# Kernel tuning notes

Hardware: AMD Instinct MI355X
Metric: run time of the kernel (lower is better)

Reference implementation:

```python
import jax, jax.numpy as jnp
import numpy as np

N_FFT = 1024
HOP = 256


def _hann(n):
    # torch.hann_window default is periodic
    return 0.5 * (1.0 - jnp.cos(2.0 * jnp.pi * jnp.arange(n) / n))


def _dft_kernel():
    # rfft(eye(n_fft)).T -> (n_fft//2+1, n_fft) complex, windowed along time axis
    win = _hann(N_FFT).astype(jnp.float32)
    dftm = jnp.fft.rfft(jnp.eye(N_FFT, dtype=jnp.float32), axis=-1).T * win[None, :]
    # rearrange 'f n ri -> (ri f) n': real rows first, then imag rows
    ker = jnp.concatenate([dftm.real, dftm.imag], axis=0)  # (2*(n_fft//2+1), n_fft)
    f2 = ker.shape[0]
    scale = jnp.ones((f2,), dtype=jnp.float32)
    scale = scale.at[1:(N_FFT + 1) // 2].set(2.0)   # positive freqs (real part), excl. DC & Nyquist
    scale = scale.at[(N_FFT + 2) // 2:].set(2.0)    # imag rows
    return (ker * scale[:, None] / N_FFT).astype(jnp.float32)  # (1026, 1024)


def setup_inputs() -> dict:
    key = jax.random.key(0)
    B, F, T = 16, N_FFT // 2 + 1, 1024
    x = jax.random.normal(key, (B, F, T, 2), dtype=jnp.float32)
    return {"x": x}


def reference(x) -> jnp.ndarray:
    # x: (B, freq, n_frames, 2)
    B, F, T, _ = x.shape
    # '... freq n ri -> ... (ri freq) n'
    xc = jnp.concatenate([x[..., 0], x[..., 1]], axis=1)  # (B, 2F, T)
    ker = _dft_kernel()                                   # (2F, n_fft)
    # conv_transpose1d(stride=hop) == per-frame GEMM then overlap-add
    frames = jnp.einsum('bct,cn->btn', xc, ker)           # (B, T, n_fft)
    L = (T - 1) * HOP + N_FFT
    idx = (jnp.arange(T)[:, None] * HOP + jnp.arange(N_FFT)[None, :]).reshape(-1)
    wav = jnp.zeros((B, L), dtype=x.dtype).at[:, idx].add(frames.reshape(B, -1))
    # COLA normalization: * hop / sum(window^2)
    win = _hann(N_FFT)
    coeff = (HOP / jnp.sum(win ** 2)).astype(x.dtype)
    return wav * coeff
```

## Files before the change

### kernel.cpp

```cpp
#include <hip/hip_runtime.h>
#include <hip/hip_bf16.h>

#define HOP 256
#define NB 16
#define NT 1024
#define MM (NB*NT)
#define LOUT ((NT-1)*HOP + 1024)
#define CQ (2.0f/(3.0f*1024.0f))
#define PACK_BLOCKS 2048

typedef __bf16 bf16x8 __attribute__((ext_vector_type(8)));
typedef float f32x4 __attribute__((ext_vector_type(4)));

__device__ __forceinline__ void gload_lds16(const void* g, void* l) {
  __builtin_amdgcn_global_load_lds(
      (const __attribute__((address_space(1))) void*)g,
      (__attribute__((address_space(3))) void*)l, 16, 0, 0);
}

__global__ void prep(const float* __restrict__ x, __hip_bfloat16* __restrict__ A,
                     __hip_bfloat16* __restrict__ B3, float* __restrict__ wint) {
  int tid = threadIdx.x;
  if (blockIdx.x >= PACK_BLOCKS) {
    int idx = (blockIdx.x - PACK_BLOCKS) * 256 + tid;
    int row = idx >> 9, c = idx & 511;
    int i = row & 255, nt = row >> 8;
    int oddh = i >> 7;
    int j = nt * 128 + (i & 127);
    int f, isSin;
    if (!oddh) {
      if (c < 257) { f = 2 * c; isSin = 0; } else { f = 2 * (c - 256); isSin = 1; }
    } else {
      if (c < 256) { f = 2 * c + 1; isSin = 0; } else { f = 2 * (c - 256) + 1; isSin = 1; }
    }
    const float w0 = 6.283185307179586f / 1024.f;
    int ph = (f * j) & 1023;
    float si, co;
    __sincosf((float)ph * w0, &si, &co);
    float sc = (f == 0 || f == 512) ? 1.f : 2.f;
    B3[idx] = __float2bfloat16(isSin ? -si * sc : co * sc);
    if (idx < 1024)
      wint[idx] = (0.5f - 0.5f * __cosf((float)idx * w0)) * CQ;
    return;
  }
  __shared__ float2 tile[64][65];
  int w = blockIdx.x;
  int b = w >> 7, fy = (w >> 4) & 7, tx = w & 15;
  int f0 = fy * 64, t0 = tx * 64;
  int tl = tid & 63, th = tid >> 6;
#pragma unroll
  for (int r = 0; r < 16; ++r) {
    int fl = r * 4 + th;
    tile[fl][tl] = *(const float2*)(x + (((size_t)b * 513 + f0 + fl) * 1024 + (t0 + tl)) * 2);
  }
  __syncthreads();
  int row = tid >> 2, s = tid & 3;
  float sp = 0.f;
  if (fy == 0 && s == 1)
    sp = x[(((size_t)b * 513 + 512) * 1024 + t0 + row) * 2];
  int cbase = (s & 1) * 256 + (s >> 1) * 512 + f0 / 2;
#pragma unroll
  for (int v = 0; v < 4; ++v) {
    bf16x8 pv;
#pragma unroll
    for (int u = 0; u < 8; ++u) {
      int e = v * 8 + u;
      float2 tv = tile[2 * e + (s >> 1)][row];
      float val = (s & 1) ? tv.y : tv.x;
      if (fy == 0 && s == 1 && e == 0) val = sp;
      pv[u] = (__bf16)val;
    }
    *(bf16x8*)(A + (size_t)(b * 1024 + t0 + row) * 1024 + cbase + v * 8) = pv;
  }
}

__global__ __launch_bounds__(512, 1) void gemm8(
    const __hip_bfloat16* __restrict__ A, const __hip_bfloat16* __restrict__ B3,
    const float* __restrict__ wint, __hip_bfloat16* __restrict__ C) {
  __shared__ __align__(16) __hip_bfloat16 smem[65536];
  int tid = threadIdx.x, lane = tid & 63, wv = tid >> 6;
  int wr = wv >> 2, wc = wv & 3;
  int nf = (blockIdx.x & 7) * 32 + (blockIdx.x >> 3);
  int M0 = (nf & 63) * 256;
  int nt = nf >> 6;
  int j0 = nt * 128;

  __hip_bfloat16* sA0 = smem;
  __hip_bfloat16* sA1 = smem + 16384;
  __hip_bfloat16* sB0 = smem + 32768;
  __hip_bfloat16* sB1 = smem + 40960;

  f32x4 accE[8][2] = {};
  f32x4 accO[8][2] = {};

#define SGA(KT, G, LB)                                                         \
  {                                                                            \
    int r_ = (G) * 64 + (tid >> 3);                                            \
    int s_ = (((tid & 7) ^ (r_ & 7)) * 8);                                     \
    gload_lds16(A + (size_t)(M0 + r_) * 1024 + (KT) * 64 + s_,                 \
                (LB) + (G) * 4096 + tid * 8);                                  \
  }
#define SGB(KT, G, LB)                                                         \
  {                                                                            \
    int r_ = (G) * 64 + (tid >> 3);                                            \
    int s_ = (((tid & 7) ^ (r_ & 7)) * 8);                                     \
    gload_lds16(B3 + (size_t)(nt * 256 + ((KT) >= 8 ? 128 : 0) + r_) * 512 +   \
                    ((KT) & 7) * 64 + s_,                                      \
                (LB) + (G) * 4096 + tid * 8);                                  \
  }
#define VMCNT(N) asm volatile("s_waitcnt vmcnt(" #N ")" ::: "memory")
#define BAR() __builtin_amdgcn_s_barrier()

#define LOADA(CA, P)                                                           \
  _Pragma("unroll") for (int jj = 0; jj < 4; ++jj) {                           \
    int row = wr * 128 + (P) * 64 + jj * 16 + (lane & 15);                     \
    _Pragma("unroll") for (int ks = 0; ks < 2; ++ks)                           \
        af[jj][ks] = *(const bf16x8*)&(CA)[row * 64 +                          \
            (((ks * 4 + (lane >> 4)) ^ (row & 7)) * 8)];                       \
  }
#define MFMAH(ACC, P)                                                          \
  __builtin_amdgcn_s_setprio(1);                                               \
  _Pragma("unroll") for (int jj = 0; jj < 4; ++jj)                             \
  _Pragma("unroll") for (int ks = 0; ks < 2; ++ks)                             \
  _Pragma("unroll") for (int ni = 0; ni < 2; ++ni)                             \
      ACC[(P) * 4 + jj][ni] = __builtin_amdgcn_mfma_f32_16x16x32_bf16(         \
          af[jj][ks], bfr[ks][ni], ACC[(P) * 4 + jj][ni], 0, 0, 0);            \
  __builtin_amdgcn_s_setprio(0);

#define TILE(CA, CB, NA, NBUF, K1, DOST, ACC)                                  \
  {                                                                            \
    bf16x8 bfr[2][2], af[4][2];                                                \
    _Pragma("unroll") for (int ni = 0; ni < 2; ++ni) {                         \
      int row = wc * 32 + ni * 16 + (lane & 15);                               \
      _Pragma("unroll") for (int ks = 0; ks < 2; ++ks)                         \
          bfr[ks][ni] = *(const bf16x8*)&(CB)[row * 64 +                       \
              (((ks * 4 + (lane >> 4)) ^ (row & 7)) * 8)];                     \
    }                                                                          \
    LOADA(CA, 0);                                                              \
    if (DOST) { SGB(K1, 0, NBUF); SGB(K1, 1, NBUF); }                          \
    BAR(); MFMAH(ACC, 0);                                                      \
    if (DOST) { VMCNT(2); } else { VMCNT(0); }                                 \
    BAR();                                                                     \
    LOADA(CA, 1);                                                              \
    if (DOST) { SGA(K1, 0, NA); SGA(K1, 2, NA); SGA(K1, 1, NA); SGA(K1, 3, NA); } \
    BAR(); MFMAH(ACC, 1);                                                      \
    if (DOST) { VMCNT(2); }                                                    \
    BAR();                                                                     \
  }

  SGB(0, 0, sB0); SGB(0, 1, sB0);
  SGA(0, 0, sA0); SGA(0, 2, sA0);
  SGA(0, 1, sA0); SGA(0, 3, sA0);
  VMCNT(2);
  BAR();

#pragma unroll
  for (int tt = 0; tt < 4; ++tt) {
    TILE(sA0, sB0, sA1, sB1, 2 * tt + 1, 1, accE);
    TILE(sA1, sB1, sA0, sB0, 2 * tt + 2, 1, accE);
  }
#pragma unroll
  for (int tt = 0; tt < 4; ++tt) {
    TILE(sA0, sB0, sA1, sB1, 2 * tt + 9, 1, accO);
    TILE(sA1, sB1, sA0, sB0, 2 * tt + 10, (tt < 3) ? 1 : 0, accO);
  }

  __hip_bfloat16* ct = smem;
  float wE[2], wO[2];
#pragma unroll
  for (int ni = 0; ni < 2; ++ni) {
    int jcol = j0 + wc * 32 + ni * 16 + (lane & 15);
    wE[ni] = wint[jcol];
    wO[ni] = wint[jcol + 512];
  }
#pragma unroll
  for (int mi = 0; mi < 8; ++mi) {
    int rbase = wr * 128 + mi * 16 + (lane >> 4) * 4;
#pragma unroll
    for (int ni = 0; ni < 2; ++ni) {
      int lc = wc * 32 + ni * 16 + (lane & 15);
#pragma unroll
      for (int r = 0; r < 4; ++r) {
        float E = accE[mi][ni][r], O = accO[mi][ni][r];
        ct[(rbase + r) * 256 + lc] = __float2bfloat16(wE[ni] * (E + O));
        ct[(rbase + r) * 256 + 128 + lc] = __float2bfloat16(wO[ni] * (E - O));
      }
    }
  }
  BAR();
#pragma unroll
  for (int k = 0; k < 16; ++k) {
    int row = k * 16 + (tid >> 5);
    int c0 = (tid & 31) * 8;
    int gcol = (c0 < 128) ? (j0 + c0) : (512 + j0 + c0 - 128);
    *(int4*)(C + (size_t)(M0 + row) * 1024 + gcol) = *(const int4*)&ct[row * 256 + c0];
  }
#undef SGA
#undef SGB
#undef VMCNT
#undef BAR
#undef LOADA
#undef MFMAH
#undef TILE
}

__global__ void ola2(const __hip_bfloat16* __restrict__ C, float* __restrict__ out) {
  int q = blockIdx.x;
  int b = blockIdx.y * 8 + (threadIdx.x >> 5);
  int r0 = (threadIdx.x & 31) * 8;
  size_t outl = (size_t)b * LOUT + q * 256 + r0;
  if (q >= 3 && q < 1024) {
    size_t mrow = ((size_t)b * 1024 + q) * 1024;
    bf16x8 v0 = *(const bf16x8*)&C[mrow + r0];
    bf16x8 v1 = *(const bf16x8*)&C[mrow - 1024 + 256 + r0];
    bf16x8 v2 = *(const bf16x8*)&C[mrow - 2048 + 512 + r0];
    bf16x8 v3 = *(const bf16x8*)&C[mrow - 3072 + 768 + r0];
    float res[8];
#pragma unroll
    for (int e = 0; e < 8; ++e)
      res[e] = (float)v0[e] + (float)v1[e] + (float)v2[e] + (float)v3[e];
    *(float4*)(out + outl) = make_float4(res[0], res[1], res[2], res[3]);
    *(float4*)(out + outl + 4) = make_float4(res[4], res[5], res[6], res[7]);
    return;
  }
#pragma unroll
  for (int e = 0; e < 8; ++e) {
    int l = q * 256 + r0 + e;
    int thi = l >> 8; if (thi > 1023) thi = 1023;
    int tlo = (l - 768) >> 8; if (tlo < 0) tlo = 0;
    float s = 0.f;
    for (int t = tlo; t <= thi; ++t)
      s += __bfloat162float(C[((size_t)b * 1024 + t) * 1024 + (l - (t << 8))]);
    out[outl + e] = s;
  }
}

extern "C" void kernel_launch(void* const* d_in, const int* in_sizes, int n_in,
                              void* d_out, int out_size, void* d_ws, size_t ws_size,
                              hipStream_t stream) {
  (void)in_sizes; (void)n_in; (void)out_size; (void)ws_size;
  const float* x = (const float*)d_in[0];
  float* out = (float*)d_out;
  char* ws = (char*)d_ws;
  size_t oA  = 0;
  size_t oB3 = oA + (size_t)MM * 1024 * 2;
  size_t oW  = oB3 + (size_t)1024 * 512 * 2;
  size_t oC  = oW + 1024 * 4;
  __hip_bfloat16* A  = (__hip_bfloat16*)(ws + oA);
  __hip_bfloat16* B3 = (__hip_bfloat16*)(ws + oB3);
  float* wint = (float*)(ws + oW);
  __hip_bfloat16* C  = (__hip_bfloat16*)(ws + oC);

  prep<<<dim3(PACK_BLOCKS + 2048), dim3(256), 0, stream>>>(x, A, B3, wint);
  gemm8<<<dim3(256), dim3(512), 0, stream>>>(A, B3, wint, C);
  ola2<<<dim3(1027, 2), dim3(256), 0, stream>>>(C, out);
}
```

Baseline: 64.11 us.

## Halve GEMM M-tile to 128 rows and launch 512 blocks with higher occupancy

```diff
diff --git a/kernel.cpp b/kernel.cpp
--- a/kernel.cpp
+++ b/kernel.cpp
@@ -74,24 +74,25 @@
   }
 }
 
-__global__ __launch_bounds__(512, 1) void gemm8(
+__global__ __launch_bounds__(512, 4) void gemm8(
     const __hip_bfloat16* __restrict__ A, const __hip_bfloat16* __restrict__ B3,
     const float* __restrict__ wint, __hip_bfloat16* __restrict__ C) {
-  __shared__ __align__(16) __hip_bfloat16 smem[65536];
+  __shared__ __align__(16) __hip_bfloat16 smem[32768];
   int tid = threadIdx.x, lane = tid & 63, wv = tid >> 6;
   int wr = wv >> 2, wc = wv & 3;
-  int nf = (blockIdx.x & 7) * 32 + (blockIdx.x >> 3);
-  int M0 = (nf & 63) * 256;
-  int nt = nf >> 6;
+  int q = blockIdx.x >> 3, xcd = blockIdx.x & 7;
+  int m_ = xcd + 8 * (q >> 2);
+  int nt = q & 3;
+  int M0 = m_ * 128;
   int j0 = nt * 128;
 
   __hip_bfloat16* sA0 = smem;
-  __hip_bfloat16* sA1 = smem + 16384;
-  __hip_bfloat16* sB0 = smem + 32768;
-  __hip_bfloat16* sB1 = smem + 40960;
-
-  f32x4 accE[8][2] = {};
-  f32x4 accO[8][2] = {};
+  __hip_bfloat16* sA1 = smem + 8192;
+  __hip_bfloat16* sB0 = smem + 16384;
+  __hip_bfloat16* sB1 = smem + 24576;
+
+  f32x4 accE[4][2] = {};
+  f32x4 accO[4][2] = {};
 
 #define SGA(KT, G, LB)                                                         \
   {                                                                            \
@@ -108,27 +109,13 @@
                     ((KT) & 7) * 64 + s_,                                      \
                 (LB) + (G) * 4096 + tid * 8);                                  \
   }
-#define VMCNT(N) asm volatile("s_waitcnt vmcnt(" #N ")" ::: "memory")
+#define VMCNT0() asm volatile("s_waitcnt vmcnt(0)" ::: "memory")
 #define BAR() __builtin_amdgcn_s_barrier()
-
-#define LOADA(CA, P)                                                           \
-  _Pragma("unroll") for (int jj = 0; jj < 4; ++jj) {                           \
-    int row = wr * 128 + (P) * 64 + jj * 16 + (lane & 15);                     \
-    _Pragma("unroll") for (int ks = 0; ks < 2; ++ks)                           \
-        af[jj][ks] = *(const bf16x8*)&(CA)[row * 64 +                          \
-            (((ks * 4 + (lane >> 4)) ^ (row & 7)) * 8)];                       \
-  }
-#define MFMAH(ACC, P)                                                          \
-  __builtin_amdgcn_s_setprio(1);                                               \
-  _Pragma("unroll") for (int jj = 0; jj < 4; ++jj)                             \
-  _Pragma("unroll") for (int ks = 0; ks < 2; ++ks)                             \
-  _Pragma("unroll") for (int ni = 0; ni < 2; ++ni)                             \
-      ACC[(P) * 4 + jj][ni] = __builtin_amdgcn_mfma_f32_16x16x32_bf16(         \
-          af[jj][ks], bfr[ks][ni], ACC[(P) * 4 + jj][ni], 0, 0, 0);            \
-  __builtin_amdgcn_s_setprio(0);
 
 #define TILE(CA, CB, NA, NBUF, K1, DOST, ACC)                                  \
   {                                                                            \
+    if (DOST) { SGB(K1, 0, NBUF); SGB(K1, 1, NBUF);                            \
+                SGA(K1, 0, NA);   SGA(K1, 1, NA); }                            \
     bf16x8 bfr[2][2], af[4][2];                                                \
     _Pragma("unroll") for (int ni = 0; ni < 2; ++ni) {                         \
       int row = wc * 32 + ni * 16 + (lane & 15);                               \
@@ -136,22 +123,26 @@
           bfr[ks][ni] = *(const bf16x8*)&(CB)[row * 64 +                       \
               (((ks * 4 + (lane >> 4)) ^ (row & 7)) * 8)];                     \
     }                                                                          \
-    LOADA(CA, 0);                                                              \
-    if (DOST) { SGB(K1, 0, NBUF); SGB(K1, 1, NBUF); }                          \
-    BAR(); MFMAH(ACC, 0);                                                      \
-    if (DOST) { VMCNT(2); } else { VMCNT(0); }                                 \
+    _Pragma("unroll") for (int mi = 0; mi < 4; ++mi) {                         \
+      int row = wr * 64 + mi * 16 + (lane & 15);                               \
+      _Pragma("unroll") for (int ks = 0; ks < 2; ++ks)                         \
+          af[mi][ks] = *(const bf16x8*)&(CA)[row * 64 +                        \
+              (((ks * 4 + (lane >> 4)) ^ (row & 7)) * 8)];                     \
+    }                                                                          \
+    __builtin_amdgcn_s_setprio(1);                                             \
+    _Pragma("unroll") for (int mi = 0; mi < 4; ++mi)                           \
+    _Pragma("unroll") for (int ks = 0; ks < 2; ++ks)                           \
+    _Pragma("unroll") for (int ni = 0; ni < 2; ++ni)                           \
+        ACC[mi][ni] = __builtin_amdgcn_mfma_f32_16x16x32_bf16(                 \
+            af[mi][ks], bfr[ks][ni], ACC[mi][ni], 0, 0, 0);                    \
+    __builtin_amdgcn_s_setprio(0);                                             \
+    VMCNT0();                                                                  \
     BAR();                                                                     \
-    LOADA(CA, 1);                                                              \
-    if (DOST) { SGA(K1, 0, NA); SGA(K1, 2, NA); SGA(K1, 1, NA); SGA(K1, 3, NA); } \
-    BAR(); MFMAH(ACC, 1);                                                      \
-    if (DOST) { VMCNT(2); }                                                    \
-    BAR();                                                                     \
   }
 
   SGB(0, 0, sB0); SGB(0, 1, sB0);
-  SGA(0, 0, sA0); SGA(0, 2, sA0);
-  SGA(0, 1, sA0); SGA(0, 3, sA0);
-  VMCNT(2);
+  SGA(0, 0, sA0); SGA(0, 1, sA0);
+  VMCNT0();
   BAR();
 
 #pragma unroll
@@ -174,8 +165,8 @@
     wO[ni] = wint[jcol + 512];
   }
 #pragma unroll
-  for (int mi = 0; mi < 8; ++mi) {
-    int rbase = wr * 128 + mi * 16 + (lane >> 4) * 4;
+  for (int mi = 0; mi < 4; ++mi) {
+    int rbase = wr * 64 + mi * 16 + (lane >> 4) * 4;
 #pragma unroll
     for (int ni = 0; ni < 2; ++ni) {
       int lc = wc * 32 + ni * 16 + (lane & 15);
@@ -189,7 +180,7 @@
   }
   BAR();
 #pragma unroll
-  for (int k = 0; k < 16; ++k) {
+  for (int k = 0; k < 8; ++k) {
     int row = k * 16 + (tid >> 5);
     int c0 = (tid & 31) * 8;
     int gcol = (c0 < 128) ? (j0 + c0) : (512 + j0 + c0 - 128);
@@ -197,10 +188,8 @@
   }
 #undef SGA
 #undef SGB
-#undef VMCNT
+#undef VMCNT0
 #undef BAR
-#undef LOADA
-#undef MFMAH
 #undef TILE
 }
 
@@ -252,6 +241,6 @@
   __hip_bfloat16* C  = (__hip_bfloat16*)(ws + oC);
 
   prep<<<dim3(PACK_BLOCKS + 2048), dim3(256), 0, stream>>>(x, A, B3, wint);
-  gemm8<<<dim3(256), dim3(512), 0, stream>>>(A, B3, wint, C);
+  gemm8<<<dim3(512), dim3(512), 0, stream>>>(A, B3, wint, C);
   ola2<<<dim3(1027, 2), dim3(256), 0, stream>>>(C, out);
 }
```

New measurement: 60.92 us. 5.0% less time.

## Split GEMM into separate even/odd halves and move butterfly and window into OLA

Applied to the files above, without the earlier changes.

```diff
diff --git a/kernel.cpp b/kernel.cpp
--- a/kernel.cpp
+++ b/kernel.cpp
@@ -24,11 +24,9 @@
   if (blockIdx.x >= PACK_BLOCKS) {
     int idx = (blockIdx.x - PACK_BLOCKS) * 256 + tid;
     int row = idx >> 9, c = idx & 511;
-    int i = row & 255, nt = row >> 8;
-    int oddh = i >> 7;
-    int j = nt * 128 + (i & 127);
+    int eo = row >> 9, j = row & 511;
     int f, isSin;
-    if (!oddh) {
+    if (!eo) {
       if (c < 257) { f = 2 * c; isSin = 0; } else { f = 2 * (c - 256); isSin = 1; }
     } else {
       if (c < 256) { f = 2 * c + 1; isSin = 0; } else { f = 2 * (c - 256) + 1; isSin = 1; }
@@ -76,115 +74,106 @@
 
 __global__ __launch_bounds__(512, 1) void gemm8(
     const __hip_bfloat16* __restrict__ A, const __hip_bfloat16* __restrict__ B3,
-    const float* __restrict__ wint, __hip_bfloat16* __restrict__ C) {
+    __hip_bfloat16* __restrict__ Craw) {
   __shared__ __align__(16) __hip_bfloat16 smem[65536];
   int tid = threadIdx.x, lane = tid & 63, wv = tid >> 6;
   int wr = wv >> 2, wc = wv & 3;
-  int nf = (blockIdx.x & 7) * 32 + (blockIdx.x >> 3);
-  int M0 = (nf & 63) * 256;
-  int nt = nf >> 6;
-  int j0 = nt * 128;
+  int xcd = blockIdx.x & 7, g = blockIdx.x >> 3;
+  int m_ = xcd + 8 * (g >> 2);
+  int sub = g & 3;
+  int eo = sub >> 1, ntile = sub & 1;
+  int M0 = m_ * 256;
+  int j0 = ntile * 256;
+  int acol = eo * 512;
+  int brow = eo * 512 + j0;
 
   __hip_bfloat16* sA0 = smem;
   __hip_bfloat16* sA1 = smem + 16384;
   __hip_bfloat16* sB0 = smem + 32768;
-  __hip_bfloat16* sB1 = smem + 40960;
-
-  f32x4 accE[8][2] = {};
-  f32x4 accO[8][2] = {};
-
-#define SGA(KT, G, LB)                                                         \
+  __hip_bfloat16* sB1 = smem + 49152;
+
+  f32x4 acc[8][4] = {};
+
+#define SG(X, RB, RS, CB, KT, G, LB)                                           \
   {                                                                            \
     int r_ = (G) * 64 + (tid >> 3);                                            \
     int s_ = (((tid & 7) ^ (r_ & 7)) * 8);                                     \
-    gload_lds16(A + (size_t)(M0 + r_) * 1024 + (KT) * 64 + s_,                 \
+    gload_lds16((X) + (size_t)((RB) + r_) * (RS) + (CB) + (KT) * 64 + s_,      \
                 (LB) + (G) * 4096 + tid * 8);                                  \
   }
-#define SGB(KT, G, LB)                                                         \
-  {                                                                            \
-    int r_ = (G) * 64 + (tid >> 3);                                            \
-    int s_ = (((tid & 7) ^ (r_ & 7)) * 8);                                     \
-    gload_lds16(B3 + (size_t)(nt * 256 + ((KT) >= 8 ? 128 : 0) + r_) * 512 +   \
-                    ((KT) & 7) * 64 + s_,                                      \
-                (LB) + (G) * 4096 + tid * 8);                                  \
-  }
+#define SGA(KT, G, LB) SG(A, M0, 1024, acol, KT, G, LB)
+#define SGB(KT, G, LB) SG(B3, brow, 512, 0, KT, G, LB)
 #define VMCNT(N) asm volatile("s_waitcnt vmcnt(" #N ")" ::: "memory")
 #define BAR() __builtin_amdgcn_s_barrier()
 
-#define LOADA(CA, P)                                                           \
-  _Pragma("unroll") for (int jj = 0; jj < 4; ++jj) {                           \
-    int row = wr * 128 + (P) * 64 + jj * 16 + (lane & 15);                     \
+#define LOADA(CA, Q)                                                           \
+  _Pragma("unroll") for (int j = 0; j < 2; ++j) {                              \
+    int row = wr * 128 + (2 * (Q) + j) * 16 + (lane & 15);                     \
     _Pragma("unroll") for (int ks = 0; ks < 2; ++ks)                           \
-        af[jj][ks] = *(const bf16x8*)&(CA)[row * 64 +                          \
+        af[j][ks] = *(const bf16x8*)&(CA)[row * 64 +                           \
             (((ks * 4 + (lane >> 4)) ^ (row & 7)) * 8)];                       \
   }
-#define MFMAH(ACC, P)                                                          \
+#define MFMAQ(Q)                                                               \
   __builtin_amdgcn_s_setprio(1);                                               \
-  _Pragma("unroll") for (int jj = 0; jj < 4; ++jj)                             \
+  _Pragma("unroll") for (int j = 0; j < 2; ++j)                                \
   _Pragma("unroll") for (int ks = 0; ks < 2; ++ks)                             \
-  _Pragma("unroll") for (int ni = 0; ni < 2; ++ni)                             \
-      ACC[(P) * 4 + jj][ni] = __builtin_amdgcn_mfma_f32_16x16x32_bf16(         \
-          af[jj][ks], bfr[ks][ni], ACC[(P) * 4 + jj][ni], 0, 0, 0);            \
+  _Pragma("unroll") for (int ni = 0; ni < 4; ++ni)                             \
+      acc[2 * (Q) + j][ni] = __builtin_amdgcn_mfma_f32_16x16x32_bf16(          \
+          af[j][ks], bfr[ks][ni], acc[2 * (Q) + j][ni], 0, 0, 0);              \
   __builtin_amdgcn_s_setprio(0);
 
-#define TILE(CA, CB, NA, NBUF, K1, DOST, ACC)                                  \
+#define TILE(CA, CB, NA, NBUF, K1, DOST)                                       \
   {                                                                            \
-    bf16x8 bfr[2][2], af[4][2];                                                \
-    _Pragma("unroll") for (int ni = 0; ni < 2; ++ni) {                         \
-      int row = wc * 32 + ni * 16 + (lane & 15);                               \
+    bf16x8 bfr[2][4], af[2][2];                                                \
+    _Pragma("unroll") for (int ni = 0; ni < 4; ++ni) {                         \
+      int row = wc * 64 + ni * 16 + (lane & 15);                               \
       _Pragma("unroll") for (int ks = 0; ks < 2; ++ks)                         \
           bfr[ks][ni] = *(const bf16x8*)&(CB)[row * 64 +                       \
               (((ks * 4 + (lane >> 4)) ^ (row & 7)) * 8)];                     \
     }                                                                          \
     LOADA(CA, 0);                                                              \
     if (DOST) { SGB(K1, 0, NBUF); SGB(K1, 1, NBUF); }                          \
-    BAR(); MFMAH(ACC, 0);                                                      \
-    if (DOST) { VMCNT(2); } else { VMCNT(0); }                                 \
+    BAR(); MFMAQ(0); BAR();                                                    \
+    LOADA(CA, 1);                                                              \
+    if (DOST) { SGB(K1, 2, NBUF); SGB(K1, 3, NBUF); }                          \
+    BAR(); MFMAQ(1);                                                           \
+    if (DOST) { VMCNT(4); } else { VMCNT(0); }                                 \
     BAR();                                                                     \
-    LOADA(CA, 1);                                                              \
-    if (DOST) { SGA(K1, 0, NA); SGA(K1, 2, NA); SGA(K1, 1, NA); SGA(K1, 3, NA); } \
-    BAR(); MFMAH(ACC, 1);                                                      \
+    LOADA(CA, 2);                                                              \
+    if (DOST) { SGA(K1, 0, NA); SGA(K1, 2, NA); }                              \
+    BAR(); MFMAQ(2); BAR();                                                    \
+    LOADA(CA, 3);                                                              \
+    if (DOST) { SGA(K1, 1, NA); SGA(K1, 3, NA); }                              \
+    BAR(); MFMAQ(3);                                                           \
     if (DOST) { VMCNT(2); }                                                    \
     BAR();                                                                     \
   }
 
   SGB(0, 0, sB0); SGB(0, 1, sB0);
+  SGB(0, 2, sB0); SGB(0, 3, sB0);
   SGA(0, 0, sA0); SGA(0, 2, sA0);
   SGA(0, 1, sA0); SGA(0, 3, sA0);
   VMCNT(2);
   BAR();
 
 #pragma unroll
-  for (int tt = 0; tt < 4; ++tt) {
-    TILE(sA0, sB0, sA1, sB1, 2 * tt + 1, 1, accE);
-    TILE(sA1, sB1, sA0, sB0, 2 * tt + 2, 1, accE);
-  }
-#pragma unroll
-  for (int tt = 0; tt < 4; ++tt) {
-    TILE(sA0, sB0, sA1, sB1, 2 * tt + 9, 1, accO);
-    TILE(sA1, sB1, sA0, sB0, 2 * tt + 10, (tt < 3) ? 1 : 0, accO);
-  }
+  for (int tt = 0; tt < 3; ++tt) {
+    TILE(sA0, sB0, sA1, sB1, 2 * tt + 1, 1);
+    TILE(sA1, sB1, sA0, sB0, 2 * tt + 2, 1);
+  }
+  TILE(sA0, sB0, sA1, sB1, 7, 1);
+  TILE(sA1, sB1, sA0, sB0, 0, 0);
 
   __hip_bfloat16* ct = smem;
-  float wE[2], wO[2];
-#pragma unroll
-  for (int ni = 0; ni < 2; ++ni) {
-    int jcol = j0 + wc * 32 + ni * 16 + (lane & 15);
-    wE[ni] = wint[jcol];
-    wO[ni] = wint[jcol + 512];
-  }
 #pragma unroll
   for (int mi = 0; mi < 8; ++mi) {
     int rbase = wr * 128 + mi * 16 + (lane >> 4) * 4;
 #pragma unroll
-    for (int ni = 0; ni < 2; ++ni) {
-      int lc = wc * 32 + ni * 16 + (lane & 15);
-#pragma unroll
-      for (int r = 0; r < 4; ++r) {
-        float E = accE[mi][ni][r], O = accO[mi][ni][r];
-        ct[(rbase + r) * 256 + lc] = __float2bfloat16(wE[ni] * (E + O));
-        ct[(rbase + r) * 256 + 128 + lc] = __float2bfloat16(wO[ni] * (E - O));
-      }
+    for (int ni = 0; ni < 4; ++ni) {
+      int col = wc * 64 + ni * 16 + (lane & 15);
+#pragma unroll
+      for (int r = 0; r < 4; ++r)
+        ct[(rbase + r) * 256 + col] = __float2bfloat16(acc[mi][ni][r]);
     }
   }
   BAR();
@@ -192,33 +181,48 @@
   for (int k = 0; k < 16; ++k) {
     int row = k * 16 + (tid >> 5);
     int c0 = (tid & 31) * 8;
-    int gcol = (c0 < 128) ? (j0 + c0) : (512 + j0 + c0 - 128);
-    *(int4*)(C + (size_t)(M0 + row) * 1024 + gcol) = *(const int4*)&ct[row * 256 + c0];
-  }
+    *(int4*)(Craw + (size_t)(M0 + row) * 1024 + eo * 512 + j0 + c0) =
+        *(const int4*)&ct[row * 256 + c0];
+  }
+#undef SG
 #undef SGA
 #undef SGB
 #undef VMCNT
 #undef BAR
 #undef LOADA
-#undef MFMAH
+#undef MFMAQ
 #undef TILE
 }
 
-__global__ void ola2(const __hip_bfloat16* __restrict__ C, float* __restrict__ out) {
+__global__ void ola2(const __hip_bfloat16* __restrict__ C, const float* __restrict__ wint,
+                     float* __restrict__ out) {
   int q = blockIdx.x;
   int b = blockIdx.y * 8 + (threadIdx.x >> 5);
   int r0 = (threadIdx.x & 31) * 8;
   size_t outl = (size_t)b * LOUT + q * 256 + r0;
   if (q >= 3 && q < 1024) {
-    size_t mrow = ((size_t)b * 1024 + q) * 1024;
-    bf16x8 v0 = *(const bf16x8*)&C[mrow + r0];
-    bf16x8 v1 = *(const bf16x8*)&C[mrow - 1024 + 256 + r0];
-    bf16x8 v2 = *(const bf16x8*)&C[mrow - 2048 + 512 + r0];
-    bf16x8 v3 = *(const bf16x8*)&C[mrow - 3072 + 768 + r0];
+    size_t m0 = ((size_t)b * 1024 + q) * 1024;
+    bf16x8 e0 = *(const bf16x8*)&C[m0 + r0];
+    bf16x8 o0 = *(const bf16x8*)&C[m0 + 512 + r0];
+    bf16x8 e1 = *(const bf16x8*)&C[m0 - 1024 + 256 + r0];
+    bf16x8 o1 = *(const bf16x8*)&C[m0 - 1024 + 768 + r0];
+    bf16x8 e2 = *(const bf16x8*)&C[m0 - 2048 + r0];
+    bf16x8 o2 = *(const bf16x8*)&C[m0 - 2048 + 512 + r0];
+    bf16x8 e3 = *(const bf16x8*)&C[m0 - 3072 + 256 + r0];
+    bf16x8 o3 = *(const bf16x8*)&C[m0 - 3072 + 768 + r0];
+    float wv[4][8];
+#pragma unroll
+    for (int h = 0; h < 4; ++h) {
+      *(float4*)&wv[h][0] = *(const float4*)&wint[h * 256 + r0];
+      *(float4*)&wv[h][4] = *(const float4*)&wint[h * 256 + r0 + 4];
+    }
     float res[8];
 #pragma unroll
     for (int e = 0; e < 8; ++e)
-      res[e] = (float)v0[e] + (float)v1[e] + (float)v2[e] + (float)v3[e];
+      res[e] = wv[0][e] * ((float)e0[e] + (float)o0[e])
+             + wv[1][e] * ((float)e1[e] + (float)o1[e])
+             + wv[2][e] * ((float)e2[e] - (float)o2[e])
+             + wv[3][e] * ((float)e3[e] - (float)o3[e]);
     *(float4*)(out + outl) = make_float4(res[0], res[1], res[2], res[3]);
     *(float4*)(out + outl + 4) = make_float4(res[4], res[5], res[6], res[7]);
     return;
@@ -229,8 +233,16 @@
     int thi = l >> 8; if (thi > 1023) thi = 1023;
     int tlo = (l - 768) >> 8; if (tlo < 0) tlo = 0;
     float s = 0.f;
-    for (int t = tlo; t <= thi; ++t)
-      s += __bfloat162float(C[((size_t)b * 1024 + t) * 1024 + (l - (t << 8))]);
+    for (int t = tlo; t <= thi; ++t) {
+      int j = l - (t << 8);
+      size_t m = ((size_t)b * 1024 + t) * 1024;
+      float fr;
+      if (j < 512)
+        fr = wint[j] * (__bfloat162float(C[m + j]) + __bfloat162float(C[m + 512 + j]));
+      else
+        fr = wint[j] * (__bfloat162float(C[m + j - 512]) - __bfloat162float(C[m + j]));
+      s += fr;
+    }
     out[outl + e] = s;
   }
 }
@@ -249,9 +261,9 @@
   __hip_bfloat16* A  = (__hip_bfloat16*)(ws + oA);
   __hip_bfloat16* B3 = (__hip_bfloat16*)(ws + oB3);
   float* wint = (float*)(ws + oW);
-  __hip_bfloat16* C  = (__hip_bfloat16*)(ws + oC);
+  __hip_bfloat16* Craw = (__hip_bfloat16*)(ws + oC);
 
   prep<<<dim3(PACK_BLOCKS + 2048), dim3(256), 0, stream>>>(x, A, B3, wint);
-  gemm8<<<dim3(256), dim3(512), 0, stream>>>(A, B3, wint, C);
-  ola2<<<dim3(1027, 2), dim3(256), 0, stream>>>(C, out);
-}
+  gemm8<<<dim3(256), dim3(512), 0, stream>>>(A, B3, Craw);
+  ola2<<<dim3(1027, 2), dim3(256), 0, stream>>>(Craw, wint, out);
+}
```

After: 64.82 us. No clear change (+1.1%).
